# Performance work log

Hardware: AMD Instinct MI355X
Metric: run time of the kernel (lower is better)

## Reference

```python
import jax, jax.numpy as jnp
import numpy as np

B, T, C = 2, 2048, 2048
N_HEAD, N_KV_HEAD, HEAD_DIM = 16, 4, 128
N_REP = N_HEAD // N_KV_HEAD
EPS = 1e-05


def setup_inputs() -> dict:
    key = jax.random.key(0)
    ks = jax.random.split(key, 8)
    # rope freqs as cos/sin of theta_t,i = t / 10000^(2i/d)
    inv_freq = 1.0 / (10000.0 ** (np.arange(0, HEAD_DIM, 2, dtype=np.float32) / HEAD_DIM))
    ang = np.arange(T, dtype=np.float32)[:, None] * inv_freq[None, :]  # [T, HEAD_DIM//2]
    scale = 0.02
    return {
        "x": jax.random.normal(ks[0], (B, T, C), jnp.float32),
        "freqs_cos": jnp.asarray(np.cos(ang)),
        "freqs_sin": jnp.asarray(np.sin(ang)),
        "wq": jax.random.normal(ks[1], (C, N_HEAD * HEAD_DIM), jnp.float32) * scale,
        "wk": jax.random.normal(ks[2], (C, N_KV_HEAD * HEAD_DIM), jnp.float32) * scale,
        "wv": jax.random.normal(ks[3], (C, N_KV_HEAD * HEAD_DIM), jnp.float32) * scale,
        "wo": jax.random.normal(ks[4], (N_HEAD * HEAD_DIM, C), jnp.float32) * scale,
        "q_norm_w": jnp.ones((HEAD_DIM,), jnp.float32),
        "k_norm_w": jnp.ones((HEAD_DIM,), jnp.float32),
    }


def _rmsnorm(x, w):
    var = jnp.mean(jnp.square(x), axis=-1, keepdims=True)
    return x * jax.lax.rsqrt(var + EPS) * w


def _rope(x, cos, sin):
    # x: [B, T, H, D]; interpret last dim as interleaved (real, imag) pairs
    xr = x[..., 0::2]
    xi = x[..., 1::2]
    c = cos[None, :, None, :]
    s = sin[None, :, None, :]
    out_r = xr * c - xi * s
    out_i = xr * s + xi * c
    return jnp.stack([out_r, out_i], axis=-1).reshape(x.shape)


def reference(x, freqs_cos, freqs_sin, wq, wk, wv, wo, q_norm_w, k_norm_w):
    # QKV projections
    xq = (x @ wq).reshape(B, T, N_HEAD, HEAD_DIM)
    xk = (x @ wk).reshape(B, T, N_KV_HEAD, HEAD_DIM)
    xv = (x @ wv).reshape(B, T, N_KV_HEAD, HEAD_DIM)
    # optional q/k RMSNorm (use_qk_norm=True)
    xq = _rmsnorm(xq, q_norm_w)
    xk = _rmsnorm(xk, k_norm_w)
    # RoPE
    xq = _rope(xq, freqs_cos, freqs_sin)
    xk = _rope(xk, freqs_cos, freqs_sin)
    # GQA expand: each kv head repeated N_REP times contiguously
    xk = jnp.repeat(xk, N_REP, axis=2)  # [B, T, N_HEAD, D]
    xv = jnp.repeat(xv, N_REP, axis=2)
    # causal SDPA
    scores = jnp.einsum("bthd,bshd->bhts", xq, xk) / jnp.sqrt(jnp.float32(HEAD_DIM))
    causal = jnp.tril(jnp.ones((T, T), bool))
    scores = jnp.where(causal[None, None], scores, jnp.float32(-1e30))
    attn = jax.nn.softmax(scores, axis=-1)
    y = jnp.einsum("bhts,bshd->bthd", attn, xv).reshape(B, T, N_HEAD * HEAD_DIM)
    return y @ wo
```

## Files before the change

kernel.cpp:

```cpp
#include <hip/hip_runtime.h>
#include <hip/hip_bf16.h>

using u16 = unsigned short;
using u32 = unsigned int;

typedef short bf16x8 __attribute__((ext_vector_type(8)));
typedef float f32x4 __attribute__((ext_vector_type(4)));

#define AS1 __attribute__((address_space(1)))
#define AS3 __attribute__((address_space(3)))

__device__ __forceinline__ void gll16(const void* g, void* l) {
  __builtin_amdgcn_global_load_lds((const AS1 u32*)g, (AS3 u32*)l, 16, 0, 0);
}

__device__ __forceinline__ u16 f2bf(float x) {
  u32 u = __builtin_bit_cast(u32, x);
  u32 r = (u + 0x7fffu + ((u >> 16) & 1u)) >> 16;
  return (u16)r;
}
__device__ __forceinline__ u32 pk2(float lo, float hi) {
  return (u32)f2bf(lo) | ((u32)f2bf(hi) << 16);
}
__device__ __forceinline__ u16 f2bf_fast(float x) {
  __hip_bfloat16 h = __float2bfloat16(x);
  return __builtin_bit_cast(u16, h);
}

__device__ __forceinline__ void trans64(const float* __restrict__ in, u16* __restrict__ out,
                                        int R, int Cc, int bx, int by, float (*tl)[65]) {
  int c0 = bx * 64, r0 = by * 64, tid = threadIdx.x;
#pragma unroll
  for (int i = 0; i < 16; i++) {
    int idx = i * 256 + tid; int tr = idx >> 6, tc = idx & 63;
    tl[tr][tc] = in[(size_t)(r0 + tr) * Cc + c0 + tc];
  }
  __syncthreads();
#pragma unroll
  for (int i = 0; i < 16; i++) {
    int idx = i * 256 + tid; int tr = idx >> 6, tc = idx & 63;
    out[(size_t)(c0 + tr) * R + r0 + tc] = f2bf(tl[tc][tr]);
  }
}

__global__ void k_prep(const float* __restrict__ x, u16* __restrict__ xb,
                       const float* __restrict__ wq, u16* __restrict__ wqt,
                       const float* __restrict__ wk, const float* __restrict__ wv,
                       u16* __restrict__ wkvt,
                       const float* __restrict__ wo, u16* __restrict__ wot,
                       const float* __restrict__ fc, const float* __restrict__ fs,
                       float2* __restrict__ fcs) {
  __shared__ float tl[64][65];
  int gid = blockIdx.x;
  if (gid < 4096) {
    int i = gid * 256 + threadIdx.x;
    const float4* p = (const float4*)(x + (size_t)i * 8);
    float4 a = p[0], b = p[1];
    uint4 o;
    o.x = pk2(a.x, a.y); o.y = pk2(a.z, a.w);
    o.z = pk2(b.x, b.y); o.w = pk2(b.z, b.w);
    *(uint4*)(xb + (size_t)i * 8) = o;
  } else if (gid < 5120) {
    int t = gid - 4096; trans64(wq, wqt, 2048, 2048, t & 31, t >> 5, tl);
  } else if (gid < 5376) {
    int t = gid - 5120; trans64(wk, wkvt, 2048, 512, t & 7, t >> 3, tl);
  } else if (gid < 5632) {
    int t = gid - 5376; trans64(wv, wkvt + 512 * 2048, 2048, 512, t & 7, t >> 3, tl);
  } else if (gid < 6656) {
    int t = gid - 5632; trans64(wo, wot, 2048, 2048, t & 31, t >> 5, tl);
  } else {
    int base = (gid - 6656) * 2048 + threadIdx.x * 8;
#pragma unroll
    for (int j = 0; j < 8; j++) {
      int idx = base + j;
      fcs[idx] = make_float2(fc[idx], fs[idx]);
    }
  }
}

template <int MODE>
__global__ __launch_bounds__(256) void k_gemm(
    const u16* __restrict__ A, const u16* __restrict__ BT0, const u16* __restrict__ BT1,
    void* __restrict__ Cout, u16* __restrict__ Kout, u16* __restrict__ Vout, int K,
    const float* __restrict__ nwq, const float* __restrict__ nwk,
    const float2* __restrict__ fcs) {
  constexpr int NX = 16;
  constexpr int RBX = 8;
  __shared__ char lds[32768];
  char* As = lds; char* Bs = lds + 16384;
  int tid = threadIdx.x, w = tid >> 6, l = tid & 63, lg = l >> 4, ll = l & 15;
  int lid = blockIdx.y * NX + blockIdx.x;
  int xcd = lid & 7, r = lid >> 3;
  int colg = xcd & 1, rowg = xcd >> 1;
  int bxt = colg * RBX + r % RBX;
  int bm0 = (rowg * 8 + r / RBX) * 128;
  const u16* BT = BT0;
  int bn0 = bxt * 128;
  int wr = w >> 1, wc = w & 1;
  f32x4 acc[4][4] = {};
  for (int k0 = 0; k0 < K; k0 += 64) {
#pragma unroll
    for (int i = 0; i < 4; i++) {
      int base = i * 256 + (w << 6);
      int p = base + l;
      int rr = p >> 3, kc = (p & 7) ^ (rr & 7);
      gll16(A + (size_t)(bm0 + rr) * K + k0 + kc * 8, As + base * 16);
      gll16(BT + (size_t)(bn0 + rr) * K + k0 + kc * 8, Bs + base * 16);
    }
    asm volatile("s_waitcnt vmcnt(0)" ::: "memory");
    __syncthreads();
#pragma unroll
    for (int ks = 0; ks < 2; ks++) {
      bf16x8 af[4], bfr[4];
#pragma unroll
      for (int m = 0; m < 4; m++) {
        int row = 64 * wr + 16 * m + ll;
        af[m] = *(const bf16x8*)(As + row * 128 + (((lg + 4 * ks) ^ (row & 7)) << 4));
      }
#pragma unroll
      for (int n = 0; n < 4; n++) {
        int row = 64 * wc + 16 * n + ll;
        bfr[n] = *(const bf16x8*)(Bs + row * 128 + (((lg + 4 * ks) ^ (row & 7)) << 4));
      }
#pragma unroll
      for (int m = 0; m < 4; m++)
#pragma unroll
        for (int n = 0; n < 4; n++)
          acc[m][n] = __builtin_amdgcn_mfma_f32_16x16x32_bf16(af[m], bfr[n], acc[m][n], 0, 0, 0);
    }
    __syncthreads();
  }
  float* C = (float*)Cout;
#pragma unroll
  for (int m = 0; m < 4; m++)
#pragma unroll
    for (int n = 0; n < 4; n++) {
      int row = bm0 + 64 * wr + 16 * m + 4 * lg;
      int col = bn0 + 64 * wc + 16 * n + ll;
      float* cp = C + (size_t)row * 2048 + col;
#pragma unroll
      for (int r2 = 0; r2 < 4; r2++) cp[(size_t)r2 * 2048] = acc[m][n][r2];
    }
  (void)nwq; (void)nwk; (void)fcs; (void)Kout; (void)Vout;
}

__global__ __launch_bounds__(512, 2) void k_gemm_qkv(
    const u16* __restrict__ A, const u16* __restrict__ BT0, const u16* __restrict__ BT1,
    u16* __restrict__ Qout, u16* __restrict__ Kout, u16* __restrict__ Vout,
    const float* __restrict__ nwq, const float* __restrict__ nwk,
    const float2* __restrict__ fcs) {
  __shared__ char lds[98304];
  const int K = 2048;
  int tid = threadIdx.x, w = tid >> 6, l = tid & 63, lg = l >> 4, ll = l & 15;
  int wr = w >> 2, wc = w & 3;
  int lid = blockIdx.y * 24 + blockIdx.x;
  int xcd = lid & 7, r = lid >> 3;
  int colg = xcd & 1, rowg = xcd >> 1;
  int bxt = colg * 12 + r % 12;
  int bm0 = (rowg * 8 + r / 12) * 128;
  bool qpath = (bxt < 16);
  const u16* BT = qpath ? BT0 : BT1;
  int bn0 = qpath ? bxt * 128 : (bxt - 16) * 128;

  auto stage = [&](int si, int kt) {
    char* Sb = lds + si * 32768;
    int k0 = kt * 64;
#pragma unroll
    for (int i = 0; i < 2; i++) {
      int base = i * 512 + (w << 6) + ((tid >> 8) << 8);
      base = i * 512 + (w << 6);
      int c = base + l;
      int row = c >> 3, kc = (c & 7) ^ (row & 7);
      gll16(A + (size_t)(bm0 + row) * K + k0 + kc * 8, Sb + base * 16);
      gll16(BT + (size_t)(bn0 + row) * K + k0 + kc * 8, Sb + 16384 + base * 16);
    }
  };

  f32x4 acc[4][2] = {};
  stage(0, 0); stage(1, 1);
  asm volatile("s_waitcnt vmcnt(4)" ::: "memory");
  __builtin_amdgcn_s_barrier();
  __builtin_amdgcn_sched_barrier(0);

  for (int kt = 0; kt < 32; ++kt) {
    int cs = kt % 3;
    if (kt + 2 < 32) stage((kt + 2) % 3, kt + 2);
    char* As = lds + cs * 32768;
    char* Bs = As + 16384;
    __builtin_amdgcn_s_setprio(1);
#pragma unroll
    for (int ks = 0; ks < 2; ks++) {
      bf16x8 af[4], bf[2];
#pragma unroll
      for (int m = 0; m < 4; m++) {
        int row = 64 * wr + 16 * m + ll;
        af[m] = *(const bf16x8*)(As + row * 128 + (((lg + 4 * ks) ^ (row & 7)) << 4));
      }
#pragma unroll
      for (int n = 0; n < 2; n++) {
        int row = 32 * wc + 16 * n + ll;
        bf[n] = *(const bf16x8*)(Bs + row * 128 + (((lg + 4 * ks) ^ (row & 7)) << 4));
      }
#pragma unroll
      for (int m = 0; m < 4; m++)
#pragma unroll
        for (int n = 0; n < 2; n++)
          acc[m][n] = __builtin_amdgcn_mfma_f32_16x16x32_bf16(af[m], bf[n], acc[m][n], 0, 0, 0);
    }
    __builtin_amdgcn_s_setprio(0);
    if (kt + 2 < 32) {
      asm volatile("s_waitcnt vmcnt(4)" ::: "memory");
    } else {
      asm volatile("s_waitcnt vmcnt(0)" ::: "memory");
    }
    __builtin_amdgcn_s_barrier();
    __builtin_amdgcn_sched_barrier(0);
  }

  if (qpath || bn0 < 512) {
    const float* nw = qpath ? nwq : nwk;
    u16* O = qpath ? Qout : Kout;
    int ostride = qpath ? 2048 : 512;
    float outscale = qpath ? 0.12751744843f : 1.0f;
    float* ssum = (float*)lds;
    float ps[4][4];
#pragma unroll
    for (int m = 0; m < 4; m++)
#pragma unroll
      for (int r2 = 0; r2 < 4; r2++) {
        float p = 0.f;
#pragma unroll
        for (int n = 0; n < 2; n++) p += acc[m][n][r2] * acc[m][n][r2];
#pragma unroll
        for (int msk = 1; msk < 16; msk <<= 1) p += __shfl_xor(p, msk);
        ps[m][r2] = p;
      }
    if (ll == 0) {
#pragma unroll
      for (int m = 0; m < 4; m++)
#pragma unroll
        for (int r2 = 0; r2 < 4; r2++)
          ssum[wr * 256 + (16 * m + 4 * lg + r2) * 4 + wc] = ps[m][r2];
    }
    __syncthreads();
    float rs[4][4];
#pragma unroll
    for (int m = 0; m < 4; m++)
#pragma unroll
      for (int r2 = 0; r2 < 4; r2++) {
        int rowl = 16 * m + 4 * lg + r2;
        const float* sp = ssum + wr * 256 + rowl * 4;
        float tot = sp[0] + sp[1] + sp[2] + sp[3];
        rs[m][r2] = rsqrtf(tot * (1.0f / 128.0f) + 1e-5f) * outscale;
      }
#pragma unroll
    for (int m = 0; m < 4; m++)
#pragma unroll
      for (int n = 0; n < 2; n++) {
        int col = bn0 + 32 * wc + 16 * n + ll;
        int d = col & 127;
        float wgt = nw[d];
        int i = d >> 1;
#pragma unroll
        for (int r2 = 0; r2 < 4; r2++) {
          int row = bm0 + 64 * wr + 16 * m + 4 * lg + r2;
          int t = row & 2047;
          float y = acc[m][n][r2] * rs[m][r2] * wgt;
          float p = __shfl_xor(y, 1);
          float2 cs = fcs[t * 64 + i];
          float o = (ll & 1) ? (p * cs.y + y * cs.x) : (y * cs.x - p * cs.y);
          O[(size_t)row * ostride + col] = f2bf(o);
        }
      }
  } else {
    int b = bm0 >> 11, t0g = bm0 & 2047;
    int kvh = (bn0 - 512) >> 7;
    int bk = b * 4 + kvh;
#pragma unroll
    for (int m = 0; m < 4; m++)
#pragma unroll
      for (int n = 0; n < 2; n++) {
        int d = 32 * wc + 16 * n + ll;
        int tloc = 64 * wr + 16 * m + 4 * lg;
        u32 w0 = pk2(acc[m][n][0], acc[m][n][1]);
        u32 w1 = pk2(acc[m][n][2], acc[m][n][3]);
        int byte = (d * 256 + tloc * 2) ^ ((d & 7) << 4);
        *(uint2*)(lds + byte) = make_uint2(w0, w1);
      }
    __syncthreads();
    int tc = tid & 15, dbase = tid >> 4;
#pragma unroll
    for (int pass = 0; pass < 4; pass++) {
      int d = dbase + pass * 32;
      int byte = (d * 256 + tc * 16) ^ ((d & 7) << 4);
      uint4 v = *(const uint4*)(lds + byte);
      *(uint4*)(Vout + ((size_t)(bk * 128 + d)) * 2048 + t0g + tc * 8) = v;
    }
  }
}

__global__ __launch_bounds__(256, 4) void k_attn(
    const u16* __restrict__ Q, const u16* __restrict__ Kb,
    const u16* __restrict__ Vt, u16* __restrict__ Y) {
  __shared__ char lds[73728];
  char* Ps = lds + 65536;
  int tid = threadIdx.x, w = tid >> 6, l = tid & 63, lg = l >> 4, ll = l & 15;
  int fid = blockIdx.x;
  int g = fid & 7, rank = fid >> 3;
  int b = g >> 2, kvh = g & 3;
  int h = kvh * 4 + (rank & 3);
  int pairId = rank >> 2;
  const u16* Kbase = Kb + ((size_t)b * 2048) * 512 + kvh * 128;
  const u16* Vbase = Vt + ((size_t)(b * 4 + kvh) * 128) * 2048;

  const bf16x8 vones = {(short)0x3F80, (short)0x3F80, (short)0x3F80, (short)0x3F80,
                        (short)0x3F80, (short)0x3F80, (short)0x3F80, (short)0x3F80};

#pragma unroll 1
  for (int qi = 0; qi < 2; qi++) {
    int qb = qi ? (31 - pairId) : pairId;
    int q0 = qb * 64;
    bf16x8 qf[4];
    {
      int qrow = b * 2048 + q0 + 16 * w + ll;
      const u16* qp = Q + (size_t)qrow * 2048 + h * 128;
#pragma unroll
      for (int ks = 0; ks < 4; ks++) qf[ks] = *(const bf16x8*)(qp + ks * 32 + lg * 8);
    }
    f32x4 o[8] = {};
    f32x4 lacc = {};

    auto stage = [&](int bi, int k0) {
      char* Kd = lds + (bi ? 32768 : 0);
      char* Vd = lds + (bi ? 49152 : 16384);
#pragma unroll
      for (int i = 0; i < 4; i++) {
        int c = i * 256 + tid;
        int dst = (i * 256 + (w << 6)) * 16;
        int krow = c >> 4, ksrc = (c & 15) ^ (krow & 7);
        gll16(Kbase + (size_t)(k0 + krow) * 512 + ksrc * 8, Kd + dst);
        int vd = c >> 3, vsrc = (c & 7) ^ (vd & 7);
        gll16(Vbase + (size_t)vd * 2048 + k0 + vsrc * 8, Vd + dst);
      }
    };

    stage(0, 0);
    asm volatile("s_waitcnt vmcnt(0)" ::: "memory");
    __syncthreads();

    int cur = 0;
    for (int it = 0; it <= qb; ++it) {
      if (it < qb) stage(cur ^ 1, (it + 1) * 64);
      char* Ks = lds + (cur ? 32768 : 0);
      char* Vs = lds + (cur ? 49152 : 16384);
      f32x4 s[4] = {};
      __builtin_amdgcn_s_setprio(1);
#pragma unroll
      for (int ks = 0; ks < 4; ks++) {
#pragma unroll
        for (int n = 0; n < 4; n++) {
          int row = 16 * n + ll;
          bf16x8 kf = *(const bf16x8*)(Ks + ((row * 256 + (lg + 4 * ks) * 16) ^ ((row & 7) << 4)));
          s[n] = __builtin_amdgcn_mfma_f32_16x16x32_bf16(qf[ks], kf, s[n], 0, 0, 0);
        }
      }
      __builtin_amdgcn_s_setprio(0);
      if (it == qb) {
        int k0 = it * 64;
#pragma unroll
        for (int n = 0; n < 4; n++) {
          int kk = k0 + 16 * n + ll;
#pragma unroll
          for (int r = 0; r < 4; r++) {
            int qq = q0 + 16 * w + 4 * lg + r;
            if (kk > qq) s[n][r] = -1e30f;
          }
        }
      }
#pragma unroll
      for (int r = 0; r < 4; r++) {
        int prow = 4 * lg + r;
#pragma unroll
        for (int n = 0; n < 4; n++) {
          float e = exp2f(s[n][r]);
          int byte = (w << 11) + ((prow * 128 + (16 * n + ll) * 2) ^ ((prow & 7) << 4));
          *(u16*)(Ps + byte) = f2bf_fast(e);
        }
      }
      __builtin_amdgcn_s_setprio(1);
#pragma unroll
      for (int ks = 0; ks < 2; ks++) {
        bf16x8 pf = *(const bf16x8*)(Ps + (w << 11) + ((ll * 128 + (lg + 4 * ks) * 16) ^ ((ll & 7) << 4)));
        lacc = __builtin_amdgcn_mfma_f32_16x16x32_bf16(pf, vones, lacc, 0, 0, 0);
#pragma unroll
        for (int n = 0; n < 8; n++) {
          int row = 16 * n + ll;
          bf16x8 vf = *(const bf16x8*)(Vs + ((row * 128 + (lg + 4 * ks) * 16) ^ ((row & 7) << 4)));
          o[n] = __builtin_amdgcn_mfma_f32_16x16x32_bf16(pf, vf, o[n], 0, 0, 0);
        }
      }
      __builtin_amdgcn_s_setprio(0);
      asm volatile("s_waitcnt vmcnt(0)" ::: "memory");
      __syncthreads();
      cur ^= 1;
    }
    float rl[4];
#pragma unroll
    for (int r = 0; r < 4; r++) rl[r] = 1.0f / lacc[r];
#pragma unroll
    for (int n = 0; n < 8; n++) {
      int col = h * 128 + 16 * n + ll;
#pragma unroll
      for (int r = 0; r < 4; r++) {
        int trow = b * 2048 + q0 + 16 * w + 4 * lg + r;
        Y[(size_t)trow * 2048 + col] = f2bf_fast(o[n][r] * rl[r]);
      }
    }
  }
  (void)Vbase;
}

extern "C" void kernel_launch(void* const* d_in, const int* in_sizes, int n_in,
                              void* d_out, int out_size, void* d_ws, size_t ws_size,
                              hipStream_t stream) {
  const float* x   = (const float*)d_in[0];
  const float* fc  = (const float*)d_in[1];
  const float* fs  = (const float*)d_in[2];
  const float* wq  = (const float*)d_in[3];
  const float* wk  = (const float*)d_in[4];
  const float* wv  = (const float*)d_in[5];
  const float* wo  = (const float*)d_in[6];
  const float* qnw = (const float*)d_in[7];
  const float* knw = (const float*)d_in[8];
  float* out = (float*)d_out;

  const size_t MB = 1ull << 20;
  char* ws = (char*)d_ws;
  u16*    xb   = (u16*)(ws);
  u16*    wqt  = (u16*)(ws + 16 * MB);
  u16*    wkvt = (u16*)(ws + 24 * MB);
  u16*    wot  = (u16*)(ws + 28 * MB);
  u16*    Qb   = (u16*)(ws + 36 * MB);
  u16*    Kbq  = (u16*)(ws + 52 * MB);
  u16*    Vtg  = (u16*)(ws + 56 * MB);
  u16*    Yb   = (u16*)(ws + 60 * MB);
  float2* fcs  = (float2*)(ws + 76 * MB);

  hipLaunchKernelGGL(k_prep, dim3(6720), dim3(256), 0, stream,
                     x, xb, wq, wqt, wk, wv, wkvt, wo, wot, fc, fs, fcs);
  hipLaunchKernelGGL(k_gemm_qkv, dim3(24, 32), dim3(512), 0, stream,
                     xb, wqt, wkvt, Qb, Kbq, Vtg, qnw, knw, fcs);
  hipLaunchKernelGGL(k_attn, dim3(512), dim3(256), 0, stream, Qb, Kbq, Vtg, Yb);
  hipLaunchKernelGGL((k_gemm<0>), dim3(16, 32), dim3(256), 0, stream,
                     Yb, wot, (const u16*)nullptr, (void*)out, (u16*)nullptr, (u16*)nullptr, 2048,
                     nullptr, nullptr, nullptr);
}
```

Before: 207.5 us.

## Deepen QKV GEMM pipeline to 4 stages; restructure attention to 128-row tiles with triple buffering

The QKV GEMM moves from a 3-deep to a 4-deep LDS ring (128KB LDS), so more K tiles are in flight before each wait. The attention kernel drops the paired 64-row query blocks per 256-thread workgroup and instead gives each 512-thread workgroup one 128-row query block. KV tiles are staged through a 3-slot ring with partial vmcnt waits and raw barriers in place of a full drain and __syncthreads every iteration. The intent is to hide global load latency and share each KV tile across more waves. The cost is higher LDS use, which lowers occupancy, and causal work is now balanced only by block order (largest blocks first) rather than by pairing.

```diff
diff --git a/kernel.cpp b/kernel.cpp
--- a/kernel.cpp
+++ b/kernel.cpp
@@ -149,7 +149,7 @@
     u16* __restrict__ Qout, u16* __restrict__ Kout, u16* __restrict__ Vout,
     const float* __restrict__ nwq, const float* __restrict__ nwk,
     const float2* __restrict__ fcs) {
-  __shared__ char lds[98304];
+  __shared__ char lds[131072];
   const int K = 2048;
   int tid = threadIdx.x, w = tid >> 6, l = tid & 63, lg = l >> 4, ll = l & 15;
   int wr = w >> 2, wc = w & 3;
@@ -167,8 +167,7 @@
     int k0 = kt * 64;
 #pragma unroll
     for (int i = 0; i < 2; i++) {
-      int base = i * 512 + (w << 6) + ((tid >> 8) << 8);
-      base = i * 512 + (w << 6);
+      int base = i * 512 + (w << 6);
       int c = base + l;
       int row = c >> 3, kc = (c & 7) ^ (row & 7);
       gll16(A + (size_t)(bm0 + row) * K + k0 + kc * 8, Sb + base * 16);
@@ -177,14 +176,14 @@
   };
 
   f32x4 acc[4][2] = {};
-  stage(0, 0); stage(1, 1);
-  asm volatile("s_waitcnt vmcnt(4)" ::: "memory");
+  stage(0, 0); stage(1, 1); stage(2, 2);
+  asm volatile("s_waitcnt vmcnt(8)" ::: "memory");
   __builtin_amdgcn_s_barrier();
   __builtin_amdgcn_sched_barrier(0);
 
   for (int kt = 0; kt < 32; ++kt) {
-    int cs = kt % 3;
-    if (kt + 2 < 32) stage((kt + 2) % 3, kt + 2);
+    int cs = kt & 3;
+    if (kt + 3 < 32) stage((kt + 3) & 3, kt + 3);
     char* As = lds + cs * 32768;
     char* Bs = As + 16384;
     __builtin_amdgcn_s_setprio(1);
@@ -208,7 +207,9 @@
           acc[m][n] = __builtin_amdgcn_mfma_f32_16x16x32_bf16(af[m], bf[n], acc[m][n], 0, 0, 0);
     }
     __builtin_amdgcn_s_setprio(0);
-    if (kt + 2 < 32) {
+    if (kt <= 28) {
+      asm volatile("s_waitcnt vmcnt(8)" ::: "memory");
+    } else if (kt == 29) {
       asm volatile("s_waitcnt vmcnt(4)" ::: "memory");
     } else {
       asm volatile("s_waitcnt vmcnt(0)" ::: "memory");
@@ -267,8 +268,8 @@
           int t = row & 2047;
           float y = acc[m][n][r2] * rs[m][r2] * wgt;
           float p = __shfl_xor(y, 1);
-          float2 cs = fcs[t * 64 + i];
-          float o = (ll & 1) ? (p * cs.y + y * cs.x) : (y * cs.x - p * cs.y);
+          float2 cs2 = fcs[t * 64 + i];
+          float o = (ll & 1) ? (p * cs2.y + y * cs2.x) : (y * cs2.x - p * cs2.y);
           O[(size_t)row * ostride + col] = f2bf(o);
         }
       }
@@ -299,125 +300,127 @@
   }
 }
 
-__global__ __launch_bounds__(256, 4) void k_attn(
+__global__ __launch_bounds__(512, 2) void k_attn(
     const u16* __restrict__ Q, const u16* __restrict__ Kb,
     const u16* __restrict__ Vt, u16* __restrict__ Y) {
-  __shared__ char lds[73728];
-  char* Ps = lds + 65536;
+  __shared__ char lds[114688];
+  char* Ps = lds + 98304;
   int tid = threadIdx.x, w = tid >> 6, l = tid & 63, lg = l >> 4, ll = l & 15;
   int fid = blockIdx.x;
   int g = fid & 7, rank = fid >> 3;
   int b = g >> 2, kvh = g & 3;
   int h = kvh * 4 + (rank & 3);
-  int pairId = rank >> 2;
+  int qb = 15 - (rank >> 2);
+  int q0 = qb * 128;
   const u16* Kbase = Kb + ((size_t)b * 2048) * 512 + kvh * 128;
   const u16* Vbase = Vt + ((size_t)(b * 4 + kvh) * 128) * 2048;
 
   const bf16x8 vones = {(short)0x3F80, (short)0x3F80, (short)0x3F80, (short)0x3F80,
                         (short)0x3F80, (short)0x3F80, (short)0x3F80, (short)0x3F80};
 
-#pragma unroll 1
-  for (int qi = 0; qi < 2; qi++) {
-    int qb = qi ? (31 - pairId) : pairId;
-    int q0 = qb * 64;
-    bf16x8 qf[4];
-    {
-      int qrow = b * 2048 + q0 + 16 * w + ll;
-      const u16* qp = Q + (size_t)qrow * 2048 + h * 128;
-#pragma unroll
-      for (int ks = 0; ks < 4; ks++) qf[ks] = *(const bf16x8*)(qp + ks * 32 + lg * 8);
-    }
-    f32x4 o[8] = {};
-    f32x4 lacc = {};
-
-    auto stage = [&](int bi, int k0) {
-      char* Kd = lds + (bi ? 32768 : 0);
-      char* Vd = lds + (bi ? 49152 : 16384);
-#pragma unroll
-      for (int i = 0; i < 4; i++) {
-        int c = i * 256 + tid;
-        int dst = (i * 256 + (w << 6)) * 16;
-        int krow = c >> 4, ksrc = (c & 15) ^ (krow & 7);
-        gll16(Kbase + (size_t)(k0 + krow) * 512 + ksrc * 8, Kd + dst);
-        int vd = c >> 3, vsrc = (c & 7) ^ (vd & 7);
-        gll16(Vbase + (size_t)vd * 2048 + k0 + vsrc * 8, Vd + dst);
-      }
-    };
-
-    stage(0, 0);
-    asm volatile("s_waitcnt vmcnt(0)" ::: "memory");
-    __syncthreads();
-
-    int cur = 0;
-    for (int it = 0; it <= qb; ++it) {
-      if (it < qb) stage(cur ^ 1, (it + 1) * 64);
-      char* Ks = lds + (cur ? 32768 : 0);
-      char* Vs = lds + (cur ? 49152 : 16384);
-      f32x4 s[4] = {};
-      __builtin_amdgcn_s_setprio(1);
-#pragma unroll
-      for (int ks = 0; ks < 4; ks++) {
-#pragma unroll
-        for (int n = 0; n < 4; n++) {
-          int row = 16 * n + ll;
-          bf16x8 kf = *(const bf16x8*)(Ks + ((row * 256 + (lg + 4 * ks) * 16) ^ ((row & 7) << 4)));
-          s[n] = __builtin_amdgcn_mfma_f32_16x16x32_bf16(qf[ks], kf, s[n], 0, 0, 0);
+  bf16x8 qf[4];
+  {
+    int qrow = b * 2048 + q0 + 16 * w + ll;
+    const u16* qp = Q + (size_t)qrow * 2048 + h * 128;
+#pragma unroll
+    for (int ks = 0; ks < 4; ks++) qf[ks] = *(const bf16x8*)(qp + ks * 32 + lg * 8);
+  }
+  f32x4 o[8] = {};
+  f32x4 lacc = {};
+
+  auto stage = [&](int si, int k0) {
+    char* Kd = lds + si * 32768;
+    char* Vd = Kd + 16384;
+#pragma unroll
+    for (int i = 0; i < 2; i++) {
+      int base = i * 512 + (w << 6);
+      int c = base + l;
+      int dst = base * 16;
+      int krow = c >> 4, ksrc = (c & 15) ^ (krow & 7);
+      gll16(Kbase + (size_t)(k0 + krow) * 512 + ksrc * 8, Kd + dst);
+      int vd = c >> 3, vsrc = (c & 7) ^ (vd & 7);
+      gll16(Vbase + (size_t)vd * 2048 + k0 + vsrc * 8, Vd + dst);
+    }
+  };
+
+  int nt = 2 * qb + 2;
+  stage(0, 0);
+  stage(1, 64);
+  asm volatile("s_waitcnt vmcnt(4)" ::: "memory");
+  __builtin_amdgcn_s_barrier();
+  __builtin_amdgcn_sched_barrier(0);
+
+  for (int it = 0; it < nt; ++it) {
+    if (it + 2 < nt) stage((it + 2) % 3, (it + 2) * 64);
+    char* Ks = lds + (it % 3) * 32768;
+    char* Vs = Ks + 16384;
+    f32x4 s[4] = {};
+    __builtin_amdgcn_s_setprio(1);
+#pragma unroll
+    for (int ks = 0; ks < 4; ks++) {
+#pragma unroll
+      for (int n = 0; n < 4; n++) {
+        int row = 16 * n + ll;
+        bf16x8 kf = *(const bf16x8*)(Ks + ((row * 256 + (lg + 4 * ks) * 16) ^ ((row & 7) << 4)));
+        s[n] = __builtin_amdgcn_mfma_f32_16x16x32_bf16(qf[ks], kf, s[n], 0, 0, 0);
+      }
+    }
+    __builtin_amdgcn_s_setprio(0);
+    if (it >= 2 * qb) {
+      int k0 = it * 64;
+#pragma unroll
+      for (int n = 0; n < 4; n++) {
+        int kk = k0 + 16 * n + ll;
+#pragma unroll
+        for (int r = 0; r < 4; r++) {
+          int qq = q0 + 16 * w + 4 * lg + r;
+          if (kk > qq) s[n][r] = -1e30f;
         }
       }
-      __builtin_amdgcn_s_setprio(0);
-      if (it == qb) {
-        int k0 = it * 64;
-#pragma unroll
-        for (int n = 0; n < 4; n++) {
-          int kk = k0 + 16 * n + ll;
-#pragma unroll
-          for (int r = 0; r < 4; r++) {
-            int qq = q0 + 16 * w + 4 * lg + r;
-            if (kk > qq) s[n][r] = -1e30f;
-          }
-        }
-      }
-#pragma unroll
-      for (int r = 0; r < 4; r++) {
-        int prow = 4 * lg + r;
-#pragma unroll
-        for (int n = 0; n < 4; n++) {
-          float e = exp2f(s[n][r]);
-          int byte = (w << 11) + ((prow * 128 + (16 * n + ll) * 2) ^ ((prow & 7) << 4));
-          *(u16*)(Ps + byte) = f2bf_fast(e);
-        }
-      }
-      __builtin_amdgcn_s_setprio(1);
-#pragma unroll
-      for (int ks = 0; ks < 2; ks++) {
-        bf16x8 pf = *(const bf16x8*)(Ps + (w << 11) + ((ll * 128 + (lg + 4 * ks) * 16) ^ ((ll & 7) << 4)));
-        lacc = __builtin_amdgcn_mfma_f32_16x16x32_bf16(pf, vones, lacc, 0, 0, 0);
-#pragma unroll
-        for (int n = 0; n < 8; n++) {
-          int row = 16 * n + ll;
-          bf16x8 vf = *(const bf16x8*)(Vs + ((row * 128 + (lg + 4 * ks) * 16) ^ ((row & 7) << 4)));
-          o[n] = __builtin_amdgcn_mfma_f32_16x16x32_bf16(pf, vf, o[n], 0, 0, 0);
-        }
-      }
-      __builtin_amdgcn_s_setprio(0);
+    }
+#pragma unroll
+    for (int r = 0; r < 4; r++) {
+      int prow = 4 * lg + r;
+#pragma unroll
+      for (int n = 0; n < 4; n++) {
+        float e = exp2f(s[n][r]);
+        int byte = (w << 11) + ((prow * 128 + (16 * n + ll) * 2) ^ ((prow & 7) << 4));
+        *(u16*)(Ps + byte) = f2bf_fast(e);
+      }
+    }
+    __builtin_amdgcn_s_setprio(1);
+#pragma unroll
+    for (int ks = 0; ks < 2; ks++) {
+      bf16x8 pf = *(const bf16x8*)(Ps + (w << 11) + ((ll * 128 + (lg + 4 * ks) * 16) ^ ((ll & 7) << 4)));
+      lacc = __builtin_amdgcn_mfma_f32_16x16x32_bf16(pf, vones, lacc, 0, 0, 0);
+#pragma unroll
+      for (int n = 0; n < 8; n++) {
+        int row = 16 * n + ll;
+        bf16x8 vf = *(const bf16x8*)(Vs + ((row * 128 + (lg + 4 * ks) * 16) ^ ((row & 7) << 4)));
+        o[n] = __builtin_amdgcn_mfma_f32_16x16x32_bf16(pf, vf, o[n], 0, 0, 0);
+      }
+    }
+    __builtin_amdgcn_s_setprio(0);
+    if (it + 2 < nt) {
+      asm volatile("s_waitcnt vmcnt(4)" ::: "memory");
+    } else {
       asm volatile("s_waitcnt vmcnt(0)" ::: "memory");
-      __syncthreads();
-      cur ^= 1;
-    }
-    float rl[4];
-#pragma unroll
-    for (int r = 0; r < 4; r++) rl[r] = 1.0f / lacc[r];
-#pragma unroll
-    for (int n = 0; n < 8; n++) {
-      int col = h * 128 + 16 * n + ll;
-#pragma unroll
-      for (int r = 0; r < 4; r++) {
-        int trow = b * 2048 + q0 + 16 * w + 4 * lg + r;
-        Y[(size_t)trow * 2048 + col] = f2bf_fast(o[n][r] * rl[r]);
-      }
-    }
-  }
-  (void)Vbase;
+    }
+    __builtin_amdgcn_s_barrier();
+    __builtin_amdgcn_sched_barrier(0);
+  }
+  float rl[4];
+#pragma unroll
+  for (int r = 0; r < 4; r++) rl[r] = 1.0f / lacc[r];
+#pragma unroll
+  for (int n = 0; n < 8; n++) {
+    int col = h * 128 + 16 * n + ll;
+#pragma unroll
+    for (int r = 0; r < 4; r++) {
+      int trow = b * 2048 + q0 + 16 * w + 4 * lg + r;
+      Y[(size_t)trow * 2048 + col] = f2bf_fast(o[n][r] * rl[r]);
+    }
+  }
 }
 
 extern "C" void kernel_launch(void* const* d_in, const int* in_sizes, int n_in,
@@ -450,7 +453,7 @@
                      x, xb, wq, wqt, wk, wv, wkvt, wo, wot, fc, fs, fcs);
   hipLaunchKernelGGL(k_gemm_qkv, dim3(24, 32), dim3(512), 0, stream,
                      xb, wqt, wkvt, Qb, Kbq, Vtg, qnw, knw, fcs);
-  hipLaunchKernelGGL(k_attn, dim3(512), dim3(256), 0, stream, Qb, Kbq, Vtg, Yb);
+  hipLaunchKernelGGL(k_attn, dim3(512), dim3(512), 0, stream, Qb, Kbq, Vtg, Yb);
   hipLaunchKernelGGL((k_gemm<0>), dim3(16, 32), dim3(256), 0, stream,
                      Yb, wot, (const u16*)nullptr, (void*)out, (u16*)nullptr, (u16*)nullptr, 2048,
                      nullptr, nullptr, nullptr);
```

Result: no change. 208.5 us (+0.5%).

## Deepen QKV GEMM pipeline to four stages and pipeline output projection GEMM

Applied to the files above, without the earlier changes.

The QKV GEMM moves from a 3-stage to a 4-stage async global-to-LDS ring buffer (128KB LDS), with the vmcnt waits adjusted to match. The simple single-buffered output-projection GEMM is replaced by a new 512-thread kernel that reuses the same 4-stage pipelined structure. The aim is to hide global load latency behind MFMA work in both GEMMs. The cost is that 128KB of LDS per block may limit how many blocks fit on a CU, against the declared launch bound of 2.

```diff
diff --git a/kernel.cpp b/kernel.cpp
--- a/kernel.cpp
+++ b/kernel.cpp
@@ -78,78 +78,12 @@
   }
 }
 
-template <int MODE>
-__global__ __launch_bounds__(256) void k_gemm(
-    const u16* __restrict__ A, const u16* __restrict__ BT0, const u16* __restrict__ BT1,
-    void* __restrict__ Cout, u16* __restrict__ Kout, u16* __restrict__ Vout, int K,
-    const float* __restrict__ nwq, const float* __restrict__ nwk,
-    const float2* __restrict__ fcs) {
-  constexpr int NX = 16;
-  constexpr int RBX = 8;
-  __shared__ char lds[32768];
-  char* As = lds; char* Bs = lds + 16384;
-  int tid = threadIdx.x, w = tid >> 6, l = tid & 63, lg = l >> 4, ll = l & 15;
-  int lid = blockIdx.y * NX + blockIdx.x;
-  int xcd = lid & 7, r = lid >> 3;
-  int colg = xcd & 1, rowg = xcd >> 1;
-  int bxt = colg * RBX + r % RBX;
-  int bm0 = (rowg * 8 + r / RBX) * 128;
-  const u16* BT = BT0;
-  int bn0 = bxt * 128;
-  int wr = w >> 1, wc = w & 1;
-  f32x4 acc[4][4] = {};
-  for (int k0 = 0; k0 < K; k0 += 64) {
-#pragma unroll
-    for (int i = 0; i < 4; i++) {
-      int base = i * 256 + (w << 6);
-      int p = base + l;
-      int rr = p >> 3, kc = (p & 7) ^ (rr & 7);
-      gll16(A + (size_t)(bm0 + rr) * K + k0 + kc * 8, As + base * 16);
-      gll16(BT + (size_t)(bn0 + rr) * K + k0 + kc * 8, Bs + base * 16);
-    }
-    asm volatile("s_waitcnt vmcnt(0)" ::: "memory");
-    __syncthreads();
-#pragma unroll
-    for (int ks = 0; ks < 2; ks++) {
-      bf16x8 af[4], bfr[4];
-#pragma unroll
-      for (int m = 0; m < 4; m++) {
-        int row = 64 * wr + 16 * m + ll;
-        af[m] = *(const bf16x8*)(As + row * 128 + (((lg + 4 * ks) ^ (row & 7)) << 4));
-      }
-#pragma unroll
-      for (int n = 0; n < 4; n++) {
-        int row = 64 * wc + 16 * n + ll;
-        bfr[n] = *(const bf16x8*)(Bs + row * 128 + (((lg + 4 * ks) ^ (row & 7)) << 4));
-      }
-#pragma unroll
-      for (int m = 0; m < 4; m++)
-#pragma unroll
-        for (int n = 0; n < 4; n++)
-          acc[m][n] = __builtin_amdgcn_mfma_f32_16x16x32_bf16(af[m], bfr[n], acc[m][n], 0, 0, 0);
-    }
-    __syncthreads();
-  }
-  float* C = (float*)Cout;
-#pragma unroll
-  for (int m = 0; m < 4; m++)
-#pragma unroll
-    for (int n = 0; n < 4; n++) {
-      int row = bm0 + 64 * wr + 16 * m + 4 * lg;
-      int col = bn0 + 64 * wc + 16 * n + ll;
-      float* cp = C + (size_t)row * 2048 + col;
-#pragma unroll
-      for (int r2 = 0; r2 < 4; r2++) cp[(size_t)r2 * 2048] = acc[m][n][r2];
-    }
-  (void)nwq; (void)nwk; (void)fcs; (void)Kout; (void)Vout;
-}
-
 __global__ __launch_bounds__(512, 2) void k_gemm_qkv(
     const u16* __restrict__ A, const u16* __restrict__ BT0, const u16* __restrict__ BT1,
     u16* __restrict__ Qout, u16* __restrict__ Kout, u16* __restrict__ Vout,
     const float* __restrict__ nwq, const float* __restrict__ nwk,
     const float2* __restrict__ fcs) {
-  __shared__ char lds[98304];
+  __shared__ char lds[131072];
   const int K = 2048;
   int tid = threadIdx.x, w = tid >> 6, l = tid & 63, lg = l >> 4, ll = l & 15;
   int wr = w >> 2, wc = w & 3;
@@ -167,8 +101,7 @@
     int k0 = kt * 64;
 #pragma unroll
     for (int i = 0; i < 2; i++) {
-      int base = i * 512 + (w << 6) + ((tid >> 8) << 8);
-      base = i * 512 + (w << 6);
+      int base = i * 512 + (w << 6);
       int c = base + l;
       int row = c >> 3, kc = (c & 7) ^ (row & 7);
       gll16(A + (size_t)(bm0 + row) * K + k0 + kc * 8, Sb + base * 16);
@@ -177,14 +110,14 @@
   };
 
   f32x4 acc[4][2] = {};
-  stage(0, 0); stage(1, 1);
-  asm volatile("s_waitcnt vmcnt(4)" ::: "memory");
+  stage(0, 0); stage(1, 1); stage(2, 2);
+  asm volatile("s_waitcnt vmcnt(8)" ::: "memory");
   __builtin_amdgcn_s_barrier();
   __builtin_amdgcn_sched_barrier(0);
 
   for (int kt = 0; kt < 32; ++kt) {
-    int cs = kt % 3;
-    if (kt + 2 < 32) stage((kt + 2) % 3, kt + 2);
+    int cs = kt & 3;
+    if (kt + 3 < 32) stage((kt + 3) & 3, kt + 3);
     char* As = lds + cs * 32768;
     char* Bs = As + 16384;
     __builtin_amdgcn_s_setprio(1);
@@ -208,7 +141,9 @@
           acc[m][n] = __builtin_amdgcn_mfma_f32_16x16x32_bf16(af[m], bf[n], acc[m][n], 0, 0, 0);
     }
     __builtin_amdgcn_s_setprio(0);
-    if (kt + 2 < 32) {
+    if (kt <= 28) {
+      asm volatile("s_waitcnt vmcnt(8)" ::: "memory");
+    } else if (kt == 29) {
       asm volatile("s_waitcnt vmcnt(4)" ::: "memory");
     } else {
       asm volatile("s_waitcnt vmcnt(0)" ::: "memory");
@@ -267,8 +202,8 @@
           int t = row & 2047;
           float y = acc[m][n][r2] * rs[m][r2] * wgt;
           float p = __shfl_xor(y, 1);
-          float2 cs = fcs[t * 64 + i];
-          float o = (ll & 1) ? (p * cs.y + y * cs.x) : (y * cs.x - p * cs.y);
+          float2 cs2 = fcs[t * 64 + i];
+          float o = (ll & 1) ? (p * cs2.y + y * cs2.x) : (y * cs2.x - p * cs2.y);
           O[(size_t)row * ostride + col] = f2bf(o);
         }
       }
@@ -297,6 +232,87 @@
       *(uint4*)(Vout + ((size_t)(bk * 128 + d)) * 2048 + t0g + tc * 8) = v;
     }
   }
+}
+
+__global__ __launch_bounds__(512, 2) void k_gemm_o(
+    const u16* __restrict__ A, const u16* __restrict__ BT, float* __restrict__ C) {
+  __shared__ char lds[131072];
+  const int K = 2048;
+  int tid = threadIdx.x, w = tid >> 6, l = tid & 63, lg = l >> 4, ll = l & 15;
+  int wr = w >> 2, wc = w & 3;
+  int lid = blockIdx.y * 16 + blockIdx.x;
+  int xcd = lid & 7, r = lid >> 3;
+  int colg = xcd & 1, rowg = xcd >> 1;
+  int bxt = colg * 8 + r % 8;
+  int bm0 = (rowg * 8 + r / 8) * 128;
+  int bn0 = bxt * 128;
+
+  auto stage = [&](int si, int kt) {
+    char* Sb = lds + si * 32768;
+    int k0 = kt * 64;
+#pragma unroll
+    for (int i = 0; i < 2; i++) {
+      int base = i * 512 + (w << 6);
+      int c = base + l;
+      int row = c >> 3, kc = (c & 7) ^ (row & 7);
+      gll16(A + (size_t)(bm0 + row) * K + k0 + kc * 8, Sb + base * 16);
+      gll16(BT + (size_t)(bn0 + row) * K + k0 + kc * 8, Sb + 16384 + base * 16);
+    }
+  };
+
+  f32x4 acc[4][2] = {};
+  stage(0, 0); stage(1, 1); stage(2, 2);
+  asm volatile("s_waitcnt vmcnt(8)" ::: "memory");
+  __builtin_amdgcn_s_barrier();
+  __builtin_amdgcn_sched_barrier(0);
+
+  for (int kt = 0; kt < 32; ++kt) {
+    int cs = kt & 3;
+    if (kt + 3 < 32) stage((kt + 3) & 3, kt + 3);
+    char* As = lds + cs * 32768;
+    char* Bs = As + 16384;
+    __builtin_amdgcn_s_setprio(1);
+#pragma unroll
+    for (int ks = 0; ks < 2; ks++) {
+      bf16x8 af[4], bf[2];
+#pragma unroll
+      for (int m = 0; m < 4; m++) {
+        int row = 64 * wr + 16 * m + ll;
+        af[m] = *(const bf16x8*)(As + row * 128 + (((lg + 4 * ks) ^ (row & 7)) << 4));
+      }
+#pragma unroll
+      for (int n = 0; n < 2; n++) {
+        int row = 32 * wc + 16 * n + ll;
+        bf[n] = *(const bf16x8*)(Bs + row * 128 + (((lg + 4 * ks) ^ (row & 7)) << 4));
+      }
+#pragma unroll
+      for (int m = 0; m < 4; m++)
+#pragma unroll
+        for (int n = 0; n < 2; n++)
+          acc[m][n] = __builtin_amdgcn_mfma_f32_16x16x32_bf16(af[m], bf[n], acc[m][n], 0, 0, 0);
+    }
+    __builtin_amdgcn_s_setprio(0);
+    if (kt <= 28) {
+      asm volatile("s_waitcnt vmcnt(8)" ::: "memory");
+    } else if (kt == 29) {
+      asm volatile("s_waitcnt vmcnt(4)" ::: "memory");
+    } else {
+      asm volatile("s_waitcnt vmcnt(0)" ::: "memory");
+    }
+    __builtin_amdgcn_s_barrier();
+    __builtin_amdgcn_sched_barrier(0);
+  }
+
+#pragma unroll
+  for (int m = 0; m < 4; m++)
+#pragma unroll
+    for (int n = 0; n < 2; n++) {
+      int row = bm0 + 64 * wr + 16 * m + 4 * lg;
+      int col = bn0 + 32 * wc + 16 * n + ll;
+      float* cp = C + (size_t)row * 2048 + col;
+#pragma unroll
+      for (int r2 = 0; r2 < 4; r2++) cp[(size_t)r2 * 2048] = acc[m][n][r2];
+    }
 }
 
 __global__ __launch_bounds__(256, 4) void k_attn(
@@ -451,7 +467,5 @@
   hipLaunchKernelGGL(k_gemm_qkv, dim3(24, 32), dim3(512), 0, stream,
                      xb, wqt, wkvt, Qb, Kbq, Vtg, qnw, knw, fcs);
   hipLaunchKernelGGL(k_attn, dim3(512), dim3(256), 0, stream, Qb, Kbq, Vtg, Yb);
-  hipLaunchKernelGGL((k_gemm<0>), dim3(16, 32), dim3(256), 0, stream,
-                     Yb, wot, (const u16*)nullptr, (void*)out, (u16*)nullptr, (u16*)nullptr, 2048,
-                     nullptr, nullptr, nullptr);
-}
+  hipLaunchKernelGGL(k_gemm_o, dim3(16, 32), dim3(512), 0, stream, Yb, wot, out);
+}
```

Result: no change. 204.7 us (-1.3%).
